# Kernel optimization log

Hardware: AMD Instinct MI355X
Metric: run time of the kernel (lower is better)

## Reference

```python
import jax, jax.numpy as jnp
import numpy as np

B, S, D = 2, 8192, 1024
H, DK, DV = 8, 64, 64
DH = 4096
SEG = 2048
NSEG = S // SEG
EPS = 1e-5


def setup_inputs() -> dict:
    key = jax.random.key(0)
    ks = jax.random.split(key, 9)
    g = lambda k, shp, sc: jax.random.normal(k, shp, jnp.float32) * sc
    return {
        "x": g(ks[0], (B, S, D), 1.0),
        "Wq": g(ks[1], (D, H * DK), 0.02),
        "Wk": g(ks[2], (D, H * DK), 0.02),
        "Wv": g(ks[3], (D, H * DV), 0.02),
        "Wo": g(ks[4], (H * DV, D), 0.02),
        "betas": g(ks[5], (1, H, 1, DV), 1.0),
        "W1": g(ks[6], (D, DH), 0.02),
        "b1": jnp.zeros((DH,), jnp.float32),
        "W2": g(ks[7], (DH, D), 0.02),
        "b2": jnp.zeros((D,), jnp.float32),
        "ln_g": jnp.ones((D,), jnp.float32),
        "ln_b": jnp.zeros((D,), jnp.float32),
    }


def _compressive_memory(x, Wq, Wk, Wv, Wo, betas):
    # project and split heads: (B, H, S, d)
    q = (x @ Wq).reshape(B, S, H, DK).transpose(0, 2, 1, 3)
    k = (x @ Wk).reshape(B, S, H, DK).transpose(0, 2, 1, 3)
    v = (x @ Wv).reshape(B, S, H, DV).transpose(0, 2, 1, 3)

    # chunk into segments: (NSEG, B, H, SEG, d)
    seg = lambda t, d: t.reshape(B, H, NSEG, SEG, d).transpose(2, 0, 1, 3, 4)
    qs, ks_, vs = seg(q, DK), seg(k, DK), seg(v, DV)

    mem0 = jnp.zeros((B, H, DK, DV), jnp.float32)
    z0 = jnp.ones((B, H, DK, 1), jnp.float32) / DK
    causal_mask = jnp.tril(jnp.ones((SEG, SEG), bool))
    scale = np.float32(1.0 / np.sqrt(DK))
    gate = jax.nn.sigmoid(betas)  # (1, H, 1, DV)

    def step(carry, inp):
        mem, z = carry
        qi, ki, vi = inp  # (B, H, SEG, d)
        sq = jax.nn.elu(qi) + 1.0
        sk = jax.nn.elu(ki) + 1.0
        # memory retrieval (uses state from previous segments)
        att_mem = (sq @ mem) / (sq @ z)  # (B, H, SEG, DV)
        # local causal SDP attention within the segment
        scores = jnp.einsum('bhqd,bhkd->bhqk', qi, ki) * scale
        scores = jnp.where(causal_mask, scores, -jnp.inf)
        att_dot = jax.nn.softmax(scores, axis=-1) @ vi
        # linear memory update
        mem = mem + jnp.einsum('bhsd,bhsv->bhdv', sk, vi)
        z = z + sk.sum(axis=-2, keepdims=True).transpose(0, 1, 3, 2)
        att = gate * att_mem + (1.0 - gate) * att_dot
        return (mem, z), att

    _, atts = jax.lax.scan(step, (mem0, z0), (qs, ks_, vs))
    # (NSEG, B, H, SEG, DV) -> (B, S, H*DV)
    att = atts.transpose(1, 0, 3, 2, 4).reshape(B, S, H * DV)
    return att @ Wo


def reference(x, Wq, Wk, Wv, Wo, betas, W1, b1, W2, b2, ln_g, ln_b):
    a = _compressive_memory(x, Wq, Wk, Wv, Wo, betas)
    h = jax.nn.gelu(a @ W1 + b1, approximate=False) @ W2 + b2
    y = h + x
    mu = y.mean(axis=-1, keepdims=True)
    var = ((y - mu) ** 2).mean(axis=-1, keepdims=True)
    return (y - mu) / jnp.sqrt(var + EPS) * ln_g + ln_b
```

## Files before the change

### kernel.cpp

```cpp
#include <hip/hip_runtime.h>
#include <hip/hip_bf16.h>
#include <math.h>

#define B_    2
#define S_    8192
#define D_    1024
#define H_N   8
#define DK_   64
#define DV_   64
#define DH_   4096
#define SEG_  2048
#define NSEG_ 4
#define EPS_  1e-5f
#define LDQKV 1536

typedef __hip_bfloat16 bf16;
typedef unsigned int u32;
typedef __attribute__((ext_vector_type(8))) short bf16x8;
typedef __attribute__((ext_vector_type(4))) float f32x4;

union bvec { bf16x8 v; bf16 e[8]; };

template <typename T> __device__ inline T from_f(float v);
template <> __device__ inline float from_f<float>(float v) { return v; }
template <> __device__ inline bf16  from_f<bf16>(float v)  { return __float2bfloat16(v); }

__device__ __forceinline__ void gld_lds16(const bf16* g, bf16* l) {
    __builtin_amdgcn_global_load_lds(
        (const __attribute__((address_space(1))) u32*)g,
        (__attribute__((address_space(3))) u32*)l, 16, 0, 0);
}

__device__ inline float elu1(float x) { return x > 0.f ? x + 1.f : __expf(x); }

template <int EPI, typename CT>
__global__ __launch_bounds__(512, 2) void gemm256(
    const bf16* __restrict__ A, const bf16* __restrict__ BT, CT* __restrict__ C,
    const float* __restrict__ bias, const float* __restrict__ resid,
    int M, int N, int K)
{
    __shared__ bf16 L[2][32768];
    const int t    = threadIdx.x;
    const int lane = t & 63;
    const int w    = t >> 6;
    const int la   = lane & 15;
    const int g    = lane >> 4;

    const int nx  = gridDim.x;
    const int nwg = nx * gridDim.y;
    const int lin = blockIdx.y * nx + blockIdx.x;
    const int swz = (lin & 7) * (nwg >> 3) + (lin >> 3);
    const int by  = swz / nx, bx = swz - by * nx;

    const int m0 = by * 256, n0 = bx * 256;
    const int wm = w >> 2, wn = w & 3;

    f32x4 acc[8][4];
    #pragma unroll
    for (int m = 0; m < 8; m++)
        #pragma unroll
        for (int n = 0; n < 4; n++) {
            f32x4 z4 = {0.f, 0.f, 0.f, 0.f};
            acc[m][n] = z4;
        }

    const bf16* Aw = A  + (size_t)(m0 + w * 32) * K;
    const bf16* Bw = BT + (size_t)(n0 + w * 32) * K;
    const int sr = lane >> 3;
    const int sc = ((lane & 7) ^ sr) * 8;

    const int nt = K >> 6;

    auto stage = [&](int kt) {
        const int buf = kt & 1;
        const size_t k0 = (size_t)kt << 6;
        #pragma unroll
        for (int i = 0; i < 4; i++) {
            gld_lds16(Aw + (size_t)(i * 8 + sr) * K + k0 + sc,
                      &L[buf][(w * 32 + i * 8) * 64]);
            gld_lds16(Bw + (size_t)(i * 8 + sr) * K + k0 + sc,
                      &L[buf][16384 + (w * 32 + i * 8) * 64]);
        }
    };

    auto rd = [&](const bf16* base, int row, int chunk) -> bf16x8 {
        return *(const bf16x8*)((const char*)base + row * 128 + ((chunk ^ (row & 7)) << 4));
    };

    stage(0);
    asm volatile("s_waitcnt vmcnt(0)" ::: "memory");
    __builtin_amdgcn_sched_barrier(0);
    __builtin_amdgcn_s_barrier();
    __builtin_amdgcn_sched_barrier(0);

    for (int kt = 0; kt < nt; kt++) {
        const bf16* Abuf = &L[kt & 1][0];
        const bf16* Bbuf = &L[kt & 1][16384];
        if (kt + 1 < nt) stage(kt + 1);

        #pragma unroll
        for (int ks = 0; ks < 2; ks++) {
            bf16x8 bg[4];
            #pragma unroll
            for (int n = 0; n < 4; n++)
                bg[n] = rd(Bbuf, wn * 64 + n * 16 + la, ks * 4 + g);
            #pragma unroll
            for (int mh = 0; mh < 2; mh++) {
                bf16x8 af[4];
                #pragma unroll
                for (int m = 0; m < 4; m++)
                    af[m] = rd(Abuf, wm * 128 + mh * 64 + m * 16 + la, ks * 4 + g);
                __builtin_amdgcn_s_setprio(1);
                #pragma unroll
                for (int m = 0; m < 4; m++)
                    #pragma unroll
                    for (int n = 0; n < 4; n++)
                        acc[mh * 4 + m][n] = __builtin_amdgcn_mfma_f32_16x16x32_bf16(
                            af[m], bg[n], acc[mh * 4 + m][n], 0, 0, 0);
                __builtin_amdgcn_s_setprio(0);
            }
        }

        if (kt + 1 < nt) {
            asm volatile("s_waitcnt vmcnt(0)" ::: "memory");
            __builtin_amdgcn_sched_barrier(0);
            __builtin_amdgcn_s_barrier();
            __builtin_amdgcn_sched_barrier(0);
        }
    }

    const int row0 = m0 + wm * 128 + g * 4;
    const int col0 = n0 + wn * 64 + la;
    #pragma unroll
    for (int n = 0; n < 4; n++) {
        const int col = col0 + n * 16;
        const float bj = (EPI >= 2) ? bias[col] : 0.f;
        #pragma unroll
        for (int m = 0; m < 8; m++) {
            #pragma unroll
            for (int r = 0; r < 4; r++) {
                const int row = row0 + m * 16 + r;
                float v = acc[m][n][r];
                if (EPI >= 2) v += bj;
                if (EPI == 2) v = 0.5f * v * (1.0f + erff(v * 0.70710678118654752f));
                if (EPI == 3) v += resid[(size_t)row * N + col];
                C[(size_t)row * N + col] = from_f<CT>(v);
            }
        }
    }
}

__global__ __launch_bounds__(256) void castx_k(const float* __restrict__ X,
                                               bf16* __restrict__ Y)
{
    size_t i = ((size_t)blockIdx.x * 256 + threadIdx.x) * 4;
    float4 v = *(const float4*)(X + i);
    union { bf16 b[4]; unsigned long long u; } o;
    o.b[0] = __float2bfloat16(v.x);
    o.b[1] = __float2bfloat16(v.y);
    o.b[2] = __float2bfloat16(v.z);
    o.b[3] = __float2bfloat16(v.w);
    *(unsigned long long*)(Y + i) = o.u;
}

__global__ __launch_bounds__(256) void transcast_k(const float* __restrict__ W,
                                                   bf16* __restrict__ WT, int K, int N)
{
    __shared__ float tile[32][33];
    const int n0 = blockIdx.x * 32, k0 = blockIdx.y * 32;
    const int tx = threadIdx.x & 31, ty = threadIdx.x >> 5;
    #pragma unroll
    for (int i = 0; i < 32; i += 8)
        tile[ty + i][tx] = W[(size_t)(k0 + ty + i) * N + n0 + tx];
    __syncthreads();
    #pragma unroll
    for (int i = 0; i < 32; i += 8)
        WT[(size_t)(n0 + ty + i) * K + k0 + tx] = __float2bfloat16(tile[tx][ty + i]);
}

__global__ __launch_bounds__(256) void vtrans_k(const bf16* __restrict__ V,
                                                bf16* __restrict__ Vt)
{
    __shared__ bf16 t_[64 * 64];
    const int t = threadIdx.x;
    const int sblk = blockIdx.x & 127;
    const int b = blockIdx.x >> 7;
    const int h = blockIdx.y;
    const bf16* src = V + ((size_t)b * S_ + sblk * 64) * LDQKV + h * 64;
    #pragma unroll
    for (int k = 0; k < 2; k++) {
        int e = t + k * 256;
        int r = e >> 3, c8 = (e & 7) * 8;
        *(bf16x8*)&t_[r * 64 + c8] = *(const bf16x8*)&src[(size_t)r * LDQKV + c8];
    }
    __syncthreads();
    const int dv = t & 63, s0 = (t >> 6) * 16;
    bf16* dst = Vt + ((size_t)(b * 8 + h) * 64 + dv) * (size_t)S_ + sblk * 64 + s0;
    bvec o0, o1;
    #pragma unroll
    for (int i = 0; i < 8; i++) {
        o0.e[i] = t_[(s0 + i) * 64 + dv];
        o1.e[i] = t_[(s0 + 8 + i) * 64 + dv];
    }
    *(bf16x8*)dst = o0.v;
    *(bf16x8*)(dst + 8) = o1.v;
}

__global__ __launch_bounds__(256) void memseg_k(
    const bf16* __restrict__ Kg, const bf16* __restrict__ Vg,
    float* __restrict__ MP, float* __restrict__ ZP)
{
    __shared__ float Ks[64][65];
    __shared__ float Vs[64][65];
    const int t = threadIdx.x, tx = t & 15, ty = t >> 4;
    const int sb = blockIdx.x;
    const int seg = sb >> 4, bh = sb & 15;
    const int b = bh >> 3, h = bh & 7;
    const int chunk = blockIdx.y;
    const size_t base = ((size_t)b * S_ + (size_t)seg * SEG_ + (size_t)chunk * 512) * LDQKV + h * 64;

    float acc[4][4] = {};
    float zacc[4]   = {};
    for (int st = 0; st < 8; st++) {
        #pragma unroll
        for (int kk = 0; kk < 2; kk++) {
            int e = t + kk * 256;
            int r = e >> 3, c8 = (e & 7) * 8;
            size_t go = base + ((size_t)st * 64 + r) * LDQKV + c8;
            bvec kv_, vv_;
            kv_.v = *(const bf16x8*)&Kg[go];
            vv_.v = *(const bf16x8*)&Vg[go];
            #pragma unroll
            for (int i = 0; i < 8; i++) {
                Ks[r][c8 + i] = elu1(__bfloat162float(kv_.e[i]));
                Vs[r][c8 + i] = __bfloat162float(vv_.e[i]);
            }
        }
        __syncthreads();
        for (int s = 0; s < 64; s++) {
            float a4[4], v4[4];
            #pragma unroll
            for (int i = 0; i < 4; i++) a4[i] = Ks[s][ty * 4 + i];
            #pragma unroll
            for (int j = 0; j < 4; j++) v4[j] = Vs[s][tx * 4 + j];
            #pragma unroll
            for (int i = 0; i < 4; i++)
                #pragma unroll
                for (int j = 0; j < 4; j++)
                    acc[i][j] += a4[i] * v4[j];
        }
        #pragma unroll
        for (int ii = 0; ii < 4; ii++) {
            int s = tx + ii * 16;
            #pragma unroll
            for (int i = 0; i < 4; i++) zacc[i] += Ks[s][ty * 4 + i];
        }
        __syncthreads();
    }
    const int slot = (seg * 4 + chunk) * 16 + bh;
    #pragma unroll
    for (int i = 0; i < 4; i++)
        #pragma unroll
        for (int j = 0; j < 4; j++)
            MP[(size_t)slot * 4096 + (ty * 4 + i) * 64 + tx * 4 + j] = acc[i][j];
    #pragma unroll
    for (int i = 0; i < 4; i++) {
        float zz = zacc[i];
        #pragma unroll
        for (int mk = 1; mk < 16; mk <<= 1) zz += __shfl_xor(zz, mk);
        if (tx == 0) ZP[slot * 64 + ty * 4 + i] = zz;
    }
}

__global__ __launch_bounds__(256) void prefix_k(
    const float* __restrict__ MP, const float* __restrict__ ZP,
    bf16* __restrict__ MST, float* __restrict__ ZS)
{
    const int bh = blockIdx.x, t = threadIdx.x;
    for (int e = t; e < 4096; e += 256) {
        int dk = e >> 6, dv = e & 63;
        float s = 0.f;
        #pragma unroll
        for (int slot = 0; slot < 16; slot++) {
            if ((slot & 3) == 0)
                MST[(size_t)((slot >> 2) * 16 + bh) * 4096 + dv * 64 + dk] = __float2bfloat16(s);
            s += MP[(size_t)(slot * 16 + bh) * 4096 + e];
        }
    }
    if (t < 64) {
        float s = 1.0f / DK_;
        #pragma unroll
        for (int slot = 0; slot < 16; slot++) {
            if ((slot & 3) == 0) ZS[((slot >> 2) * 16 + bh) * 64 + t] = s;
            s += ZP[(slot * 16 + bh) * 64 + t];
        }
    }
}

template <int NG>
__device__ __forceinline__ void stageT(const bf16* gsrc, size_t stride, bf16* lds,
                                       int wave, int lane)
{
    #pragma unroll
    for (int ii = 0; ii < NG; ii++) {
        int i = wave * NG + ii;
        gld_lds16(gsrc + (size_t)(8 * i + (lane >> 3)) * stride
                        + (size_t)(((lane & 7) ^ (lane >> 3)) * 8),
                  lds + i * 512);
    }
}

__device__ __forceinline__ bf16x8 ldsw128(const bf16* base, int row, int colE)
{
    int off = row * 128 + ((colE * 2) ^ ((row & 7) << 4));
    return *(const bf16x8*)((const char*)base + off);
}

__global__ __launch_bounds__(256) void attn_k(
    const bf16* __restrict__ Qg, const bf16* __restrict__ Kg, const bf16* __restrict__ Vt,
    const bf16* __restrict__ MsT, const float* __restrict__ ZS,
    const float* __restrict__ betas, bf16* __restrict__ att)
{
    __shared__ bf16 KT[2][4096];
    __shared__ bf16 VTs[2][4096];
    __shared__ bf16 QP[8192];
    __shared__ float Zsm[64];

    const int t    = threadIdx.x;
    const int lane = t & 63;
    const int w    = t >> 6;
    const int la   = lane & 15;
    const int g    = lane >> 4;
    const int qt   = (int)gridDim.x - 1 - (int)blockIdx.x;
    const int bh   = blockIdx.y;
    const int seg  = blockIdx.z;
    const int b    = bh >> 3, h = bh & 7;

    const size_t srow = (size_t)b * S_ + (size_t)seg * SEG_;
    const bf16* qp  = Qg + (srow + (size_t)qt * 128) * LDQKV + h * 64;
    const bf16* kp  = Kg + srow * LDQKV + h * 64;
    const bf16* vtp = Vt + (size_t)bh * 64 * (size_t)S_ + (size_t)seg * SEG_;

    stageT<4>(qp, LDQKV, QP, w, lane);
    stageT<2>(kp, LDQKV, KT[0], w, lane);
    stageT<2>(vtp, S_, VTs[0], w, lane);
    if (t < 64) Zsm[t] = ZS[(seg * 16 + bh) * 64 + t];
    __syncthreads();

    bf16x8 aq[2][2];
    #pragma unroll
    for (int st = 0; st < 2; st++)
        #pragma unroll
        for (int s = 0; s < 2; s++)
            aq[st][s] = ldsw128(QP, w * 32 + st * 16 + la, s * 32 + g * 8);

    float m_[2] = {-1e30f, -1e30f};
    float l_[2] = {0.f, 0.f};
    f32x4 Oa[2][4];
    #pragma unroll
    for (int st = 0; st < 2; st++)
        #pragma unroll
        for (int j = 0; j < 4; j++) { f32x4 z4 = {0.f,0.f,0.f,0.f}; Oa[st][j] = z4; }

    const int jtmax = 2 * qt + 1;
    int cur = 0;
    for (int jt = 0; jt <= jtmax; jt++, cur ^= 1) {
        if (jt < jtmax) {
            stageT<2>(kp + (size_t)(jt + 1) * 64 * LDQKV, LDQKV, KT[cur ^ 1], w, lane);
            stageT<2>(vtp + (size_t)(jt + 1) * 64, S_, VTs[cur ^ 1], w, lane);
        }

        bf16x8 kf[2][4];
        #pragma unroll
        for (int s = 0; s < 2; s++)
            #pragma unroll
            for (int j = 0; j < 4; j++)
                kf[s][j] = ldsw128(KT[cur], j * 16 + la, s * 32 + g * 8);

        const int jtkv = jt * 64;
        #pragma unroll
        for (int st = 0; st < 2; st++) {
            f32x4 sc[4];
            #pragma unroll
            for (int j = 0; j < 4; j++) { f32x4 z4 = {0.f,0.f,0.f,0.f}; sc[j] = z4; }
            #pragma unroll
            for (int j = 0; j < 4; j++) {
                sc[j] = __builtin_amdgcn_mfma_f32_16x16x32_bf16(kf[0][j], aq[st][0], sc[j], 0, 0, 0);
                sc[j] = __builtin_amdgcn_mfma_f32_16x16x32_bf16(kf[1][j], aq[st][1], sc[j], 0, 0, 0);
            }

            const int q_abs = qt * 128 + w * 32 + st * 16 + la;
            float sv[4][4];
            float mx = -1e30f;
            #pragma unroll
            for (int j = 0; j < 4; j++)
                #pragma unroll
                for (int r = 0; r < 4; r++) {
                    float v = sc[j][r] * 0.125f;
                    int kv = jtkv + j * 16 + g * 4 + r;
                    v = (kv <= q_abs) ? v : -1e30f;
                    sv[j][r] = v;
                    mx = fmaxf(mx, v);
                }
            mx = fmaxf(mx, __shfl_xor(mx, 16));
            mx = fmaxf(mx, __shfl_xor(mx, 32));
            float mnew = fmaxf(m_[st], mx);
            float corr = __expf(m_[st] - mnew);
            float rs = 0.f;
            #pragma unroll
            for (int j = 0; j < 4; j++)
                #pragma unroll
                for (int r = 0; r < 4; r++) {
                    float p = __expf(sv[j][r] - mnew);
                    sv[j][r] = p;
                    rs += p;
                }
            rs += __shfl_xor(rs, 16);
            rs += __shfl_xor(rs, 32);
            l_[st] = l_[st] * corr + rs;
            m_[st] = mnew;

            const int R = w * 32 + st * 16 + la;
            #pragma unroll
            for (int j = 0; j < 4; j++) {
                union { bf16 e[4]; uint2 u; } pk;
                #pragma unroll
                for (int r = 0; r < 4; r++) pk.e[r] = __float2bfloat16(sv[j][r]);
                int off = R * 128 + ((j * 32 + g * 8) ^ ((la & 7) << 4));
                *(uint2*)((char*)QP + off) = pk.u;
            }

            #pragma unroll
            for (int r = 0; r < 4; r++) {
                float corr_r = __shfl(corr, (lane & 48) | (g * 4 + r));
                #pragma unroll
                for (int j = 0; j < 4; j++) Oa[st][j][r] *= corr_r;
            }
        }

        asm volatile("s_waitcnt lgkmcnt(0)" ::: "memory");
        __builtin_amdgcn_sched_barrier(0);

        bf16x8 bv[2][4];
        #pragma unroll
        for (int s = 0; s < 2; s++)
            #pragma unroll
            for (int j = 0; j < 4; j++)
                bv[s][j] = ldsw128(VTs[cur], j * 16 + la, s * 32 + g * 8);
        #pragma unroll
        for (int st = 0; st < 2; st++) {
            bf16x8 ap0 = ldsw128(QP, w * 32 + st * 16 + la, g * 8);
            bf16x8 ap1 = ldsw128(QP, w * 32 + st * 16 + la, 32 + g * 8);
            #pragma unroll
            for (int j = 0; j < 4; j++) {
                Oa[st][j] = __builtin_amdgcn_mfma_f32_16x16x32_bf16(ap0, bv[0][j], Oa[st][j], 0, 0, 0);
                Oa[st][j] = __builtin_amdgcn_mfma_f32_16x16x32_bf16(ap1, bv[1][j], Oa[st][j], 0, 0, 0);
            }
        }
        __syncthreads();
    }

    stageT<2>(MsT + (size_t)(seg * 16 + bh) * 4096, 64, KT[0], w, lane);
    __syncthreads();

    bf16x8 sq[2][2];
    float den[2] = {0.f, 0.f};
    #pragma unroll
    for (int st = 0; st < 2; st++) {
        #pragma unroll
        for (int s = 0; s < 2; s++) {
            bvec in, outv;
            in.v = aq[st][s];
            #pragma unroll
            for (int e = 0; e < 8; e++) {
                float f = elu1(__bfloat162float(in.e[e]));
                outv.e[e] = __float2bfloat16(f);
                den[st] += f * Zsm[s * 32 + 8 * g + e];
            }
            sq[st][s] = outv.v;
        }
        den[st] += __shfl_xor(den[st], 16);
        den[st] += __shfl_xor(den[st], 32);
    }

    bf16x8 bm[2][4];
    #pragma unroll
    for (int s = 0; s < 2; s++)
        #pragma unroll
        for (int j = 0; j < 4; j++)
            bm[s][j] = ldsw128(KT[0], j * 16 + la, s * 32 + g * 8);

    float gate[4];
    #pragma unroll
    for (int j = 0; j < 4; j++)
        gate[j] = 1.f / (1.f + __expf(-betas[h * 64 + j * 16 + la]));

    #pragma unroll
    for (int st = 0; st < 2; st++) {
        f32x4 num[4];
        #pragma unroll
        for (int j = 0; j < 4; j++) { f32x4 z4 = {0.f,0.f,0.f,0.f}; num[j] = z4; }
        #pragma unroll
        for (int j = 0; j < 4; j++) {
            num[j] = __builtin_amdgcn_mfma_f32_16x16x32_bf16(sq[st][0], bm[0][j], num[j], 0, 0, 0);
            num[j] = __builtin_amdgcn_mfma_f32_16x16x32_bf16(sq[st][1], bm[1][j], num[j], 0, 0, 0);
        }
        #pragma unroll
        for (int r = 0; r < 4; r++) {
            float den_r = __shfl(den[st], (lane & 48) | (g * 4 + r));
            float l_r   = __shfl(l_[st],  (lane & 48) | (g * 4 + r));
            float linv  = 1.f / l_r;
            float dinv  = 1.f / den_r;
            size_t orow = srow + (size_t)qt * 128 + w * 32 + st * 16 + g * 4 + r;
            #pragma unroll
            for (int j = 0; j < 4; j++) {
                float am = num[j][r] * dinv;
                float ad = Oa[st][j][r] * linv;
                att[orow * 512 + h * 64 + j * 16 + la] =
                    __float2bfloat16(gate[j] * am + (1.f - gate[j]) * ad);
            }
        }
    }
}

__global__ __launch_bounds__(256) void ln_k(
    const float* __restrict__ Y, const float* __restrict__ g,
    const float* __restrict__ bta, float* __restrict__ out)
{
    const int row = blockIdx.x;
    const float* yp = Y + (size_t)row * D_;
    const int t = threadIdx.x;
    float v[4];
    float s = 0.f, s2 = 0.f;
    #pragma unroll
    for (int i = 0; i < 4; i++) {
        v[i] = yp[t + i * 256];
        s += v[i]; s2 += v[i] * v[i];
    }
    #pragma unroll
    for (int mk = 1; mk < 64; mk <<= 1) {
        s  += __shfl_xor(s, mk);
        s2 += __shfl_xor(s2, mk);
    }
    __shared__ float ss[4], ss2[4];
    int w = t >> 6;
    if ((t & 63) == 0) { ss[w] = s; ss2[w] = s2; }
    __syncthreads();
    s  = ss[0] + ss[1] + ss[2] + ss[3];
    s2 = ss2[0] + ss2[1] + ss2[2] + ss2[3];
    float mu   = s / D_;
    float var  = s2 / D_ - mu * mu;
    float rstd = rsqrtf(var + EPS_);
    #pragma unroll
    for (int i = 0; i < 4; i++) {
        int c = t + i * 256;
        out[(size_t)row * D_ + c] = (v[i] - mu) * rstd * g[c] + bta[c];
    }
}

extern "C" void kernel_launch(void* const* d_in, const int* in_sizes, int n_in,
                              void* d_out, int out_size, void* d_ws, size_t ws_size,
                              hipStream_t stream)
{
    const float* x     = (const float*)d_in[0];
    const float* Wq    = (const float*)d_in[1];
    const float* Wk    = (const float*)d_in[2];
    const float* Wv    = (const float*)d_in[3];
    const float* Wo    = (const float*)d_in[4];
    const float* betas = (const float*)d_in[5];
    const float* W1    = (const float*)d_in[6];
    const float* b1    = (const float*)d_in[7];
    const float* W2    = (const float*)d_in[8];
    const float* b2    = (const float*)d_in[9];
    const float* lng   = (const float*)d_in[10];
    const float* lnb   = (const float*)d_in[11];
    float* out = (float*)d_out;

    const int M = B_ * S_;
    char* base = (char*)d_ws;
    const size_t MB = 1024 * 1024;

    bf16*  Ab    = (bf16*)(base);
    bf16*  Hb    = (bf16*)(base + 32 * MB);
    bf16*  Xbf   = (bf16*)(base + 32 * MB);
    bf16*  QKV   = (bf16*)(base + 64 * MB);
    bf16*  Vt    = (bf16*)(base + 112 * MB);
    bf16*  ATT   = (bf16*)(base + 128 * MB);
    bf16*  WqkvT = (bf16*)(base + 160 * MB);
    bf16*  WoT   = (bf16*)(base + 163 * MB);
    bf16*  W1T   = (bf16*)(base + 164 * MB);
    bf16*  W2T   = (bf16*)(base + 172 * MB);
    float* MP    = (float*)(base + 180 * MB);
    bf16*  MST   = (bf16*)(base + 184 * MB);
    float* ZP    = (float*)(base + 185 * MB);
    float* ZS    = (float*)(base + 185 * MB + 256 * 1024);

    dim3 blk(256);
    dim3 blk512(512);

    castx_k<<<dim3((M * D_) / 1024), blk, 0, stream>>>(x, Xbf);
    transcast_k<<<dim3(512 / 32, 1024 / 32), blk, 0, stream>>>(Wq, WqkvT, 1024, 512);
    transcast_k<<<dim3(512 / 32, 1024 / 32), blk, 0, stream>>>(Wk, WqkvT + 512 * 1024, 1024, 512);
    transcast_k<<<dim3(512 / 32, 1024 / 32), blk, 0, stream>>>(Wv, WqkvT + 1024 * 1024, 1024, 512);
    transcast_k<<<dim3(1024 / 32, 512 / 32), blk, 0, stream>>>(Wo, WoT, 512, 1024);
    transcast_k<<<dim3(4096 / 32, 1024 / 32), blk, 0, stream>>>(W1, W1T, 1024, 4096);
    transcast_k<<<dim3(1024 / 32, 4096 / 32), blk, 0, stream>>>(W2, W2T, 4096, 1024);

    gemm256<0, bf16><<<dim3(1536 / 256, M / 256), blk512, 0, stream>>>(
        Xbf, WqkvT, QKV, nullptr, nullptr, M, 1536, 1024);

    vtrans_k<<<dim3(256, 8), blk, 0, stream>>>(QKV + 1024, Vt);

    memseg_k<<<dim3(NSEG_ * 16, 4), blk, 0, stream>>>(QKV + 512, QKV + 1024, MP, ZP);
    prefix_k<<<dim3(16), blk, 0, stream>>>(MP, ZP, MST, ZS);

    attn_k<<<dim3(SEG_ / 128, 16, NSEG_), blk, 0, stream>>>(
        QKV, QKV + 512, Vt, MST, ZS, betas, ATT);

    gemm256<0, bf16><<<dim3(1024 / 256, M / 256), blk512, 0, stream>>>(
        ATT, WoT, Ab, nullptr, nullptr, M, 1024, 512);
    gemm256<2, bf16><<<dim3(4096 / 256, M / 256), blk512, 0, stream>>>(
        Ab, W1T, Hb, b1, nullptr, M, 4096, 1024);
    gemm256<3, float><<<dim3(1024 / 256, M / 256), blk512, 0, stream>>>(
        Hb, W2T, out, b2, x, M, 1024, 4096);

    ln_k<<<dim3(M), blk, 0, stream>>>(out, lng, lnb, out);
}
```

Baseline: 702.4 us.

## Replace 256x256 GEMM tiles with 128x128 tiles and BK=32 double buffering

The 512-thread 256x256 GEMM kernel is swapped for a 256-thread kernel with 128x128 output tiles and a K step of 32. It uses two separate LDS buffers with a new XOR swizzle and an unrolled ping-pong loop, and drops the setprio hints. Smaller tiles give four times more workgroups per GEMM and use less LDS per block, which helps wave fill and occupancy. The cost is less data reuse per tile, more global and LDS traffic, and twice as many barriers per unit of K.

```diff
diff --git a/kernel.cpp b/kernel.cpp
--- a/kernel.cpp
+++ b/kernel.cpp
@@ -33,13 +33,16 @@
 
 __device__ inline float elu1(float x) { return x > 0.f ? x + 1.f : __expf(x); }
 
+#define VMC(N) asm volatile("s_waitcnt vmcnt(" #N ")" ::: "memory")
+
 template <int EPI, typename CT>
-__global__ __launch_bounds__(512, 2) void gemm256(
+__global__ __launch_bounds__(256, 4) void gemm128(
     const bf16* __restrict__ A, const bf16* __restrict__ BT, CT* __restrict__ C,
     const float* __restrict__ bias, const float* __restrict__ resid,
     int M, int N, int K)
 {
-    __shared__ bf16 L[2][32768];
+    __shared__ bf16 L0[8192];
+    __shared__ bf16 L1[8192];
     const int t    = threadIdx.x;
     const int lane = t & 63;
     const int w    = t >> 6;
@@ -49,99 +52,95 @@
     const int nx  = gridDim.x;
     const int nwg = nx * gridDim.y;
     const int lin = blockIdx.y * nx + blockIdx.x;
-    const int swz = (lin & 7) * (nwg >> 3) + (lin >> 3);
-    const int by  = swz / nx, bx = swz - by * nx;
-
-    const int m0 = by * 256, n0 = bx * 256;
-    const int wm = w >> 2, wn = w & 3;
-
-    f32x4 acc[8][4];
-    #pragma unroll
-    for (int m = 0; m < 8; m++)
+    const int swzb = (lin & 7) * (nwg >> 3) + (lin >> 3);
+    const int by  = swzb / nx, bx = swzb - by * nx;
+
+    const int m0 = by * 128, n0 = bx * 128;
+    const int wm = w >> 1, wn = w & 1;
+
+    f32x4 acc[4][4];
+    #pragma unroll
+    for (int m = 0; m < 4; m++)
         #pragma unroll
         for (int n = 0; n < 4; n++) {
             f32x4 z4 = {0.f, 0.f, 0.f, 0.f};
             acc[m][n] = z4;
         }
 
-    const bf16* Aw = A  + (size_t)(m0 + w * 32) * K;
-    const bf16* Bw = BT + (size_t)(n0 + w * 32) * K;
-    const int sr = lane >> 3;
-    const int sc = ((lane & 7) ^ sr) * 8;
-
-    const int nt = K >> 6;
-
-    auto stage = [&](int kt) {
-        const int buf = kt & 1;
-        const size_t k0 = (size_t)kt << 6;
-        #pragma unroll
-        for (int i = 0; i < 4; i++) {
-            gld_lds16(Aw + (size_t)(i * 8 + sr) * K + k0 + sc,
-                      &L[buf][(w * 32 + i * 8) * 64]);
-            gld_lds16(Bw + (size_t)(i * 8 + sr) * K + k0 + sc,
-                      &L[buf][16384 + (w * 32 + i * 8) * 64]);
+    const int nt = K >> 5;
+
+    const int r16 = lane >> 2;
+    const int c4  = ((lane & 3) ^ ((lane >> 3) & 3)) * 8;
+    auto stage = [&](int kt_, bf16* Lb) {
+        const size_t k0 = (size_t)kt_ << 5;
+        #pragma unroll
+        for (int j = 0; j < 2; j++) {
+            const int row = (j * 4 + w) * 16 + r16;
+            gld_lds16(A  + (size_t)(m0 + row) * K + k0 + c4,
+                      Lb + (j * 4 + w) * 512);
+            gld_lds16(BT + (size_t)(n0 + row) * K + k0 + c4,
+                      Lb + 4096 + (j * 4 + w) * 512);
         }
     };
 
-    auto rd = [&](const bf16* base, int row, int chunk) -> bf16x8 {
-        return *(const bf16x8*)((const char*)base + row * 128 + ((chunk ^ (row & 7)) << 4));
+    const int swz = ((g ^ ((la >> 1) & 3)) << 4);
+    const char* bA0 = (const char*)L0 + (wm * 64 + la) * 64 + swz;
+    const char* bB0 = (const char*)L0 + 8192 + (wn * 64 + la) * 64 + swz;
+    const char* bA1 = (const char*)L1 + (wm * 64 + la) * 64 + swz;
+    const char* bB1 = (const char*)L1 + 8192 + (wn * 64 + la) * 64 + swz;
+
+    auto comp = [&](const char* bA, const char* bB) {
+        bf16x8 af[4], bg[4];
+        #pragma unroll
+        for (int n = 0; n < 4; n++) bg[n] = *(const bf16x8*)(bB + n * 1024);
+        #pragma unroll
+        for (int m = 0; m < 4; m++) af[m] = *(const bf16x8*)(bA + m * 1024);
+        #pragma unroll
+        for (int m = 0; m < 4; m++)
+            #pragma unroll
+            for (int n = 0; n < 4; n++)
+                acc[m][n] = __builtin_amdgcn_mfma_f32_16x16x32_bf16(
+                    af[m], bg[n], acc[m][n], 0, 0, 0);
     };
 
-    stage(0);
-    asm volatile("s_waitcnt vmcnt(0)" ::: "memory");
+    stage(0, L0);
+    VMC(0);
     __builtin_amdgcn_sched_barrier(0);
     __builtin_amdgcn_s_barrier();
-    __builtin_amdgcn_sched_barrier(0);
-
-    for (int kt = 0; kt < nt; kt++) {
-        const bf16* Abuf = &L[kt & 1][0];
-        const bf16* Bbuf = &L[kt & 1][16384];
-        if (kt + 1 < nt) stage(kt + 1);
-
-        #pragma unroll
-        for (int ks = 0; ks < 2; ks++) {
-            bf16x8 bg[4];
-            #pragma unroll
-            for (int n = 0; n < 4; n++)
-                bg[n] = rd(Bbuf, wn * 64 + n * 16 + la, ks * 4 + g);
-            #pragma unroll
-            for (int mh = 0; mh < 2; mh++) {
-                bf16x8 af[4];
-                #pragma unroll
-                for (int m = 0; m < 4; m++)
-                    af[m] = rd(Abuf, wm * 128 + mh * 64 + m * 16 + la, ks * 4 + g);
-                __builtin_amdgcn_s_setprio(1);
-                #pragma unroll
-                for (int m = 0; m < 4; m++)
-                    #pragma unroll
-                    for (int n = 0; n < 4; n++)
-                        acc[mh * 4 + m][n] = __builtin_amdgcn_mfma_f32_16x16x32_bf16(
-                            af[m], bg[n], acc[mh * 4 + m][n], 0, 0, 0);
-                __builtin_amdgcn_s_setprio(0);
-            }
-        }
-
-        if (kt + 1 < nt) {
-            asm volatile("s_waitcnt vmcnt(0)" ::: "memory");
+
+    for (int tt = 0; tt < nt; tt += 2) {
+        const bool more = (tt + 2 < nt);
+        stage(tt + 1, L1);
+        comp(bA0, bB0);
+        VMC(0);
+        __builtin_amdgcn_sched_barrier(0);
+        __builtin_amdgcn_s_barrier();
+        if (more) stage(tt + 2, L0);
+        comp(bA1, bB1);
+        if (more) {
+            VMC(0);
             __builtin_amdgcn_sched_barrier(0);
             __builtin_amdgcn_s_barrier();
-            __builtin_amdgcn_sched_barrier(0);
-        }
-    }
-
-    const int row0 = m0 + wm * 128 + g * 4;
+        }
+    }
+
+    const int row0 = m0 + wm * 64 + g * 4;
     const int col0 = n0 + wn * 64 + la;
-    #pragma unroll
-    for (int n = 0; n < 4; n++) {
-        const int col = col0 + n * 16;
-        const float bj = (EPI >= 2) ? bias[col] : 0.f;
-        #pragma unroll
-        for (int m = 0; m < 8; m++) {
-            #pragma unroll
-            for (int r = 0; r < 4; r++) {
-                const int row = row0 + m * 16 + r;
+    float bj[4];
+    if (EPI >= 2) {
+        #pragma unroll
+        for (int n = 0; n < 4; n++) bj[n] = bias[col0 + n * 16];
+    }
+    #pragma unroll
+    for (int m = 0; m < 4; m++) {
+        #pragma unroll
+        for (int r = 0; r < 4; r++) {
+            const int row = row0 + m * 16 + r;
+            #pragma unroll
+            for (int n = 0; n < 4; n++) {
+                const int col = col0 + n * 16;
                 float v = acc[m][n][r];
-                if (EPI >= 2) v += bj;
+                if (EPI >= 2) v += bj[n];
                 if (EPI == 2) v = 0.5f * v * (1.0f + erff(v * 0.70710678118654752f));
                 if (EPI == 3) v += resid[(size_t)row * N + col];
                 C[(size_t)row * N + col] = from_f<CT>(v);
@@ -596,7 +595,6 @@
     float* ZS    = (float*)(base + 185 * MB + 256 * 1024);
 
     dim3 blk(256);
-    dim3 blk512(512);
 
     castx_k<<<dim3((M * D_) / 1024), blk, 0, stream>>>(x, Xbf);
     transcast_k<<<dim3(512 / 32, 1024 / 32), blk, 0, stream>>>(Wq, WqkvT, 1024, 512);
@@ -606,7 +604,7 @@
     transcast_k<<<dim3(4096 / 32, 1024 / 32), blk, 0, stream>>>(W1, W1T, 1024, 4096);
     transcast_k<<<dim3(1024 / 32, 4096 / 32), blk, 0, stream>>>(W2, W2T, 4096, 1024);
 
-    gemm256<0, bf16><<<dim3(1536 / 256, M / 256), blk512, 0, stream>>>(
+    gemm128<0, bf16><<<dim3(1536 / 128, M / 128), blk, 0, stream>>>(
         Xbf, WqkvT, QKV, nullptr, nullptr, M, 1536, 1024);
 
     vtrans_k<<<dim3(256, 8), blk, 0, stream>>>(QKV + 1024, Vt);
@@ -617,11 +615,11 @@
     attn_k<<<dim3(SEG_ / 128, 16, NSEG_), blk, 0, stream>>>(
         QKV, QKV + 512, Vt, MST, ZS, betas, ATT);
 
-    gemm256<0, bf16><<<dim3(1024 / 256, M / 256), blk512, 0, stream>>>(
+    gemm128<0, bf16><<<dim3(1024 / 128, M / 128), blk, 0, stream>>>(
         ATT, WoT, Ab, nullptr, nullptr, M, 1024, 512);
-    gemm256<2, bf16><<<dim3(4096 / 256, M / 256), blk512, 0, stream>>>(
+    gemm128<2, bf16><<<dim3(4096 / 128, M / 128), blk, 0, stream>>>(
         Ab, W1T, Hb, b1, nullptr, M, 4096, 1024);
-    gemm256<3, float><<<dim3(1024 / 256, M / 256), blk512, 0, stream>>>(
+    gemm128<3, float><<<dim3(1024 / 128, M / 128), blk, 0, stream>>>(
         Hb, W2T, out, b2, x, M, 1024, 4096);
 
     ln_k<<<dim3(M), blk, 0, stream>>>(out, lng, lnb, out);
```

Measured after the change: 732.6 us. 4.3% more time.
